# Optimization experiments

Measured on AMD Instinct MI355X. Metric: run time of the kernel, lower is better.

Reference implementation:

```python
import jax, jax.numpy as jnp
import numpy as np

N_NODES = 50000
N_EVENTS = 500000
P = 127          # previous_embed_size
A = P + 1        # agg_features
O = A + P        # w2 out size = 255
BN_EPS = 1e-5


def setup_inputs() -> dict:
    key = jax.random.key(0)
    ks = jax.random.split(key, 12)
    inp = {
        "u": jax.random.randint(ks[0], (N_EVENTS,), 0, N_NODES),
        "v": jax.random.randint(ks[1], (N_EVENTS,), 0, N_NODES),
        "g": jax.random.uniform(ks[2], (N_EVENTS, 1), dtype=jnp.float32),
        "h": jax.random.normal(ks[3], (N_NODES, P), dtype=jnp.float32),
        "remember_u": jax.random.normal(ks[4], (N_EVENTS, P), dtype=jnp.float32),
        "remember_v": jax.random.normal(ks[5], (N_EVENTS, P), dtype=jnp.float32),
        "bn_gamma": jnp.ones((A,), jnp.float32),
        "bn_beta": jnp.zeros((A,), jnp.float32),
        "w1_w": jax.random.normal(ks[6], (A, A), dtype=jnp.float32) / np.sqrt(A),
        "w1_b": jax.random.normal(ks[7], (A,), dtype=jnp.float32) * 0.01,
        "w2_w": jax.random.normal(ks[8], (O, O), dtype=jnp.float32) / np.sqrt(O),
        "w2_b": jax.random.normal(ks[9], (O,), dtype=jnp.float32) * 0.01,
        "event": N_EVENTS,
    }
    return inp


def reference(u, v, g, h, remember_u, remember_v, bn_gamma, bn_beta,
              w1_w, w1_b, w2_w, w2_b, event):
    n_nodes = h.shape[0]
    agg_feat = bn_gamma.shape[0]
    # per-edge messages: cat(stale embedding, time feature)  -> [E, A]
    src_u = jnp.concatenate([remember_u, g], axis=1)
    src_v = jnp.concatenate([remember_v, g], axis=1)
    # scatter_add into node buffers (row-wise scatter, index expanded in torch)
    agg_v = jnp.zeros((n_nodes, agg_feat), g.dtype).at[v].add(src_u)
    agg_u = jnp.zeros((n_nodes, agg_feat), g.dtype).at[u].add(src_v)
    agg = agg_u + agg_v  # [N, A]
    # BatchNorm1d (training mode: batch stats over node dim, biased var)
    mean = jnp.mean(agg, axis=0)
    var = jnp.var(agg, axis=0)
    x = (agg - mean) * jax.lax.rsqrt(var + BN_EPS) * bn_gamma + bn_beta
    # 2-layer MLP with skip-cat of h
    x1 = jax.nn.relu(x @ w1_w.T + w1_b)                 # [N, A]
    out = jnp.concatenate([h, x1], axis=1) @ w2_w.T + w2_b  # [N, A+P]
    return out
```

## Files before the change

### kernel.cpp

```cpp
#include <hip/hip_runtime.h>

constexpr int PDIM = 127;
constexpr int ADIM = 128;
constexpr int ODIM = 255;
constexpr int RTILE = 32;
constexpr int CAP = 80;
constexpr float EPS = 1e-5f;

constexpr int XS_STRIDE = 136;
constexpr int CS_STRIDE = 264;

typedef short bf16x8 __attribute__((ext_vector_type(8)));
typedef float f32x4 __attribute__((ext_vector_type(4)));

__device__ inline unsigned short f2b(float x) {
    unsigned u = __builtin_bit_cast(unsigned, x);
    u += 0x7FFF + ((u >> 16) & 1);
    return (unsigned short)(u >> 16);
}

__global__ __launch_bounds__(256) void bucket_kernel(
    const int* __restrict__ u, const int* __restrict__ v,
    const float* __restrict__ g,
    int* __restrict__ cnt, int* __restrict__ bucket,
    float* __restrict__ gsum, int E)
{
    int e = blockIdx.x * 256 + threadIdx.x;
    if (e >= E) return;
    float gv = g[e];
    int vn = v[e];
    int slot = atomicAdd(&cnt[vn], 1);
    if (slot < CAP) bucket[(long long)vn * CAP + slot] = e;
    unsafeAtomicAdd(&gsum[vn], gv);
    int un = u[e];
    slot = atomicAdd(&cnt[un], 1);
    if (slot < CAP) bucket[(long long)un * CAP + slot] = e | (1 << 20);
    unsafeAtomicAdd(&gsum[un], gv);
}

__global__ __launch_bounds__(256) void gather_kernel(
    const int* __restrict__ cnt, const int* __restrict__ bucket,
    const float* __restrict__ gsum,
    const float* __restrict__ ru, const float* __restrict__ rv,
    float* __restrict__ agg, int N)
{
    __shared__ int codes[8][CAP];
    int tid = threadIdx.x;
    int hw = tid >> 5;
    int sub = tid & 31;
    long long node = (long long)blockIdx.x * 8 + hw;
    bool valid = (node < N);
    int nd = valid ? (int)node : 0;
    int deg = valid ? cnt[nd] : 0;
    if (deg > CAP) deg = CAP;
    const int* bkt = bucket + (long long)nd * CAP;
    codes[hw][sub] = bkt[sub];
    codes[hw][32 + sub] = bkt[32 + sub];
    if (sub < CAP - 64) codes[hw][64 + sub] = bkt[64 + sub];

    int eoff = (sub < 31) ? 4 * sub : 123;
    f32x4 acc = {0.f, 0.f, 0.f, 0.f};
    int d = 0;
    for (; d + 4 <= deg; d += 4) {
        f32x4 vb[4];
        #pragma unroll
        for (int k = 0; k < 4; ++k) {
            int c = codes[hw][d + k];
            int e = c & 0xFFFFF;
            const float* s = (c & (1 << 20)) ? rv : ru;
            vb[k] = *reinterpret_cast<const f32x4*>(s + (long long)e * PDIM + eoff);
        }
        #pragma unroll
        for (int k = 0; k < 4; ++k) acc += vb[k];
    }
    for (; d < deg; ++d) {
        int c = codes[hw][d];
        int e = c & 0xFFFFF;
        const float* s = (c & (1 << 20)) ? rv : ru;
        acc += *reinterpret_cast<const f32x4*>(s + (long long)e * PDIM + eoff);
    }
    if (!valid) return;
    float* arow = agg + node * ADIM;
    if (sub < 31) {
        *reinterpret_cast<f32x4*>(arow + 4 * sub) = acc;
    } else {
        f32x4 o; o.x = acc.y; o.y = acc.z; o.z = acc.w; o.w = gsum[nd];
        *reinterpret_cast<f32x4*>(arow + 124) = o;
    }
}

__global__ __launch_bounds__(256) void colstats_kernel(
    const float* __restrict__ agg, float* __restrict__ csum,
    float* __restrict__ csumsq, int N)
{
    int j = threadIdx.x & 127;
    int rh = threadIdx.x >> 7;
    float s = 0.f, ss = 0.f;
    for (int r = blockIdx.x * 2 + rh; r < N; r += gridDim.x * 2) {
        float x = agg[(long long)r * ADIM + j];
        s += x; ss += x * x;
    }
    __shared__ float sh[2][128];
    __shared__ float sh2[2][128];
    sh[rh][j] = s; sh2[rh][j] = ss;
    __syncthreads();
    if (threadIdx.x < 128) {
        unsafeAtomicAdd(&csum[j], sh[0][j] + sh[1][j]);
        unsafeAtomicAdd(&csumsq[j], sh2[0][j] + sh2[1][j]);
    }
}

__global__ void finalize_kernel(const float* __restrict__ csum,
                                const float* __restrict__ csumsq,
                                const float* __restrict__ gamma,
                                const float* __restrict__ beta,
                                float* __restrict__ scale,
                                float* __restrict__ shift, int N)
{
    int j = threadIdx.x;
    if (j >= ADIM) return;
    float inv = 1.f / (float)N;
    float mean = csum[j] * inv;
    float var = csumsq[j] * inv - mean * mean;
    float sc = gamma[j] * rsqrtf(var + EPS);
    scale[j] = sc;
    shift[j] = beta[j] - mean * sc;
}

__global__ __launch_bounds__(256) void wprep_kernel(
    const float* __restrict__ w1, const float* __restrict__ w2,
    unsigned short* __restrict__ w1b, unsigned short* __restrict__ w2b)
{
    int t = blockIdx.x * 256 + threadIdx.x;
    if (t < 65536) {
        int o = t >> 8, k = t & 255;
        w2b[t] = (o < ODIM && k < ODIM) ? f2b(w2[o * ODIM + k]) : (unsigned short)0;
    } else {
        int s = t - 65536;
        if (s < ADIM * ADIM) w1b[s] = f2b(w1[s]);
    }
}

__global__ __launch_bounds__(256, 4) void mlp_kernel(
    const float* __restrict__ agg, const float* __restrict__ h,
    const float* __restrict__ scale, const float* __restrict__ shift,
    const unsigned short* __restrict__ w1b, const float* __restrict__ b1,
    const unsigned short* __restrict__ w2b, const float* __restrict__ b2,
    float* __restrict__ out, int N)
{
    __shared__ unsigned short xs[RTILE * XS_STRIDE];
    __shared__ unsigned short cs[RTILE * CS_STRIDE];
    int tid = threadIdx.x;
    int row0 = blockIdx.x * RTILE;
    int lane = tid & 63;
    int wave = tid >> 6;

    {
        int j = tid & 127, rh = tid >> 7;
        float sc = scale[j], sf = shift[j];
        for (int i = 0; i < RTILE / 2; ++i) {
            int r = i * 2 + rh;
            long long grow = row0 + r;
            float x = 0.f, hv = 0.f;
            if (grow < N) {
                x = agg[grow * ADIM + j] * sc + sf;
                if (j < PDIM) hv = h[grow * PDIM + j];
            }
            xs[r * XS_STRIDE + j] = f2b(x);
            cs[r * CS_STRIDE + j] = f2b(hv);
        }
        if (tid < RTILE) cs[tid * CS_STRIDE + 255] = 0;
    }
    __syncthreads();

    {
        int arow = lane & 15, akg = lane >> 4;
        bf16x8 afr[2][4];
        #pragma unroll
        for (int rt = 0; rt < 2; ++rt)
            #pragma unroll
            for (int ks = 0; ks < 4; ++ks)
                afr[rt][ks] = *reinterpret_cast<const bf16x8*>(
                    &xs[(rt * 16 + arow) * XS_STRIDE + ks * 32 + akg * 8]);
        #pragma unroll
        for (int t = 0; t < 2; ++t) {
            int bcol = (wave * 2 + t) * 16 + (lane & 15);
            bf16x8 bfr[4];
            #pragma unroll
            for (int ks = 0; ks < 4; ++ks)
                bfr[ks] = *reinterpret_cast<const bf16x8*>(&w1b[bcol * ADIM + ks * 32 + akg * 8]);
            float bias = b1[bcol];
            #pragma unroll
            for (int rt = 0; rt < 2; ++rt) {
                f32x4 acc = {0.f, 0.f, 0.f, 0.f};
                #pragma unroll
                for (int ks = 0; ks < 4; ++ks)
                    acc = __builtin_amdgcn_mfma_f32_16x16x32_bf16(afr[rt][ks], bfr[ks], acc, 0, 0, 0);
                #pragma unroll
                for (int i = 0; i < 4; ++i) {
                    int r = rt * 16 + (lane >> 4) * 4 + i;
                    float x1 = fmaxf(acc[i] + bias, 0.f);
                    cs[r * CS_STRIDE + PDIM + bcol] = f2b(x1);
                }
            }
        }
    }
    __syncthreads();

    {
        int arow = lane & 15, akg = lane >> 4;
        bf16x8 caf[2][8];
        #pragma unroll
        for (int rt = 0; rt < 2; ++rt)
            #pragma unroll
            for (int ks = 0; ks < 8; ++ks)
                caf[rt][ks] = *reinterpret_cast<const bf16x8*>(
                    &cs[(rt * 16 + arow) * CS_STRIDE + ks * 32 + akg * 8]);
        #pragma unroll
        for (int t = 0; t < 4; ++t) {
            int o = (wave * 4 + t) * 16 + (lane & 15);
            bf16x8 bfr[8];
            #pragma unroll
            for (int ks = 0; ks < 8; ++ks)
                bfr[ks] = *reinterpret_cast<const bf16x8*>(&w2b[o * 256 + ks * 32 + akg * 8]);
            float bias = (o < ODIM) ? b2[o] : 0.f;
            #pragma unroll
            for (int rt = 0; rt < 2; ++rt) {
                f32x4 acc = {0.f, 0.f, 0.f, 0.f};
                #pragma unroll
                for (int ks = 0; ks < 8; ++ks)
                    acc = __builtin_amdgcn_mfma_f32_16x16x32_bf16(caf[rt][ks], bfr[ks], acc, 0, 0, 0);
                if (o < ODIM) {
                    #pragma unroll
                    for (int i = 0; i < 4; ++i) {
                        long long grow = row0 + rt * 16 + (lane >> 4) * 4 + i;
                        if (grow < N) out[grow * ODIM + o] = acc[i] + bias;
                    }
                }
            }
        }
    }
}

extern "C" void kernel_launch(void* const* d_in, const int* in_sizes, int n_in,
                              void* d_out, int out_size, void* d_ws, size_t ws_size,
                              hipStream_t stream)
{
    const int*   u     = (const int*)d_in[0];
    const int*   v     = (const int*)d_in[1];
    const float* g     = (const float*)d_in[2];
    const float* h     = (const float*)d_in[3];
    const float* ru    = (const float*)d_in[4];
    const float* rv    = (const float*)d_in[5];
    const float* gamma = (const float*)d_in[6];
    const float* beta  = (const float*)d_in[7];
    const float* w1w   = (const float*)d_in[8];
    const float* w1b_f = (const float*)d_in[9];
    const float* w2w   = (const float*)d_in[10];
    const float* w2b_f = (const float*)d_in[11];

    int E = in_sizes[0];
    int N = in_sizes[3] / PDIM;

    int*   cnt    = (int*)d_ws;
    float* gsum   = (float*)d_ws + N;
    float* csum   = gsum + N;
    float* csumsq = csum + ADIM;
    float* scale  = csumsq + ADIM;
    float* shift  = scale + ADIM;
    int*   bucket = (int*)(shift + ADIM);
    float* agg    = (float*)(bucket + (long long)N * CAP);
    unsigned short* w1b = (unsigned short*)(agg + (long long)N * ADIM);
    unsigned short* w2b = w1b + ADIM * ADIM;

    (void)hipMemsetAsync(cnt, 0, ((size_t)(2 * N) + 2 * ADIM) * sizeof(float), stream);

    wprep_kernel<<<(65536 + ADIM * ADIM + 255) / 256, 256, 0, stream>>>(w1w, w2w, w1b, w2b);

    bucket_kernel<<<(E + 255) / 256, 256, 0, stream>>>(u, v, g, cnt, bucket, gsum, E);

    int gblocks = (N + 7) / 8;
    gather_kernel<<<gblocks, 256, 0, stream>>>(cnt, bucket, gsum, ru, rv, agg, N);

    colstats_kernel<<<1024, 256, 0, stream>>>(agg, csum, csumsq, N);
    finalize_kernel<<<1, 128, 0, stream>>>(csum, csumsq, gamma, beta, scale, shift, N);

    int mblocks = (N + RTILE - 1) / RTILE;
    mlp_kernel<<<mblocks, 256, 0, stream>>>(agg, h, scale, shift, w1b, w1b_f, w2b, w2b_f,
                                            (float*)d_out, N);
}
```

Before: 326.4 us.

## Fuse BatchNorm column statistics into gather and gather time feature per node

Column sum and sum-of-squares are now computed in the gather kernel's epilogue from register values via shared-memory reduction and atomics, removing the separate colstats pass that reread the aggregated matrix. The per-node time-feature sum is now gathered from g inside the gather loop instead of using float atomics in the bucket kernel, which also shrinks the memset. The trade-off is many more global atomics on only 256 addresses (one set per 8-node block) and an extra scattered load per edge on one lane.

```diff
diff --git a/kernel.cpp b/kernel.cpp
--- a/kernel.cpp
+++ b/kernel.cpp
@@ -21,30 +21,28 @@
 
 __global__ __launch_bounds__(256) void bucket_kernel(
     const int* __restrict__ u, const int* __restrict__ v,
-    const float* __restrict__ g,
-    int* __restrict__ cnt, int* __restrict__ bucket,
-    float* __restrict__ gsum, int E)
+    int* __restrict__ cnt, int* __restrict__ bucket, int E)
 {
     int e = blockIdx.x * 256 + threadIdx.x;
     if (e >= E) return;
-    float gv = g[e];
     int vn = v[e];
     int slot = atomicAdd(&cnt[vn], 1);
     if (slot < CAP) bucket[(long long)vn * CAP + slot] = e;
-    unsafeAtomicAdd(&gsum[vn], gv);
     int un = u[e];
     slot = atomicAdd(&cnt[un], 1);
     if (slot < CAP) bucket[(long long)un * CAP + slot] = e | (1 << 20);
-    unsafeAtomicAdd(&gsum[un], gv);
 }
 
 __global__ __launch_bounds__(256) void gather_kernel(
     const int* __restrict__ cnt, const int* __restrict__ bucket,
-    const float* __restrict__ gsum,
+    const float* __restrict__ g,
     const float* __restrict__ ru, const float* __restrict__ rv,
-    float* __restrict__ agg, int N)
+    float* __restrict__ agg, float* __restrict__ csum,
+    float* __restrict__ csumsq, int N)
 {
     __shared__ int codes[8][CAP];
+    __shared__ float ssum[8][128];
+    __shared__ float ssq[8][128];
     int tid = threadIdx.x;
     int hw = tid >> 5;
     int sub = tid & 31;
@@ -60,53 +58,63 @@
 
     int eoff = (sub < 31) ? 4 * sub : 123;
     f32x4 acc = {0.f, 0.f, 0.f, 0.f};
+    float gacc = 0.f;
+    bool g31 = (sub == 31);
     int d = 0;
     for (; d + 4 <= deg; d += 4) {
         f32x4 vb[4];
+        float gb[4];
         #pragma unroll
         for (int k = 0; k < 4; ++k) {
             int c = codes[hw][d + k];
             int e = c & 0xFFFFF;
             const float* s = (c & (1 << 20)) ? rv : ru;
             vb[k] = *reinterpret_cast<const f32x4*>(s + (long long)e * PDIM + eoff);
-        }
-        #pragma unroll
-        for (int k = 0; k < 4; ++k) acc += vb[k];
+            gb[k] = g31 ? g[e] : 0.f;
+        }
+        #pragma unroll
+        for (int k = 0; k < 4; ++k) { acc += vb[k]; gacc += gb[k]; }
     }
     for (; d < deg; ++d) {
         int c = codes[hw][d];
         int e = c & 0xFFFFF;
         const float* s = (c & (1 << 20)) ? rv : ru;
         acc += *reinterpret_cast<const f32x4*>(s + (long long)e * PDIM + eoff);
-    }
-    if (!valid) return;
-    float* arow = agg + node * ADIM;
-    if (sub < 31) {
-        *reinterpret_cast<f32x4*>(arow + 4 * sub) = acc;
+        if (g31) gacc += g[e];
+    }
+
+    int cbase = (sub < 31) ? 4 * sub : 124;
+    float v0 = (sub < 31) ? acc.x : acc.y;
+    float v1 = (sub < 31) ? acc.y : acc.z;
+    float v2 = (sub < 31) ? acc.z : acc.w;
+    float v3 = (sub < 31) ? acc.w : gacc;
+    ssum[hw][cbase + 0] = v0;  ssq[hw][cbase + 0] = v0 * v0;
+    ssum[hw][cbase + 1] = v1;  ssq[hw][cbase + 1] = v1 * v1;
+    ssum[hw][cbase + 2] = v2;  ssq[hw][cbase + 2] = v2 * v2;
+    ssum[hw][cbase + 3] = v3;  ssq[hw][cbase + 3] = v3 * v3;
+
+    if (valid) {
+        float* arow = agg + node * ADIM;
+        if (sub < 31) {
+            *reinterpret_cast<f32x4*>(arow + 4 * sub) = acc;
+        } else {
+            f32x4 o; o.x = acc.y; o.y = acc.z; o.z = acc.w; o.w = gacc;
+            *reinterpret_cast<f32x4*>(arow + 124) = o;
+        }
+    }
+
+    __syncthreads();
+    if (tid < 128) {
+        float s = 0.f;
+        #pragma unroll
+        for (int h2 = 0; h2 < 8; ++h2) s += ssum[h2][tid];
+        unsafeAtomicAdd(&csum[tid], s);
     } else {
-        f32x4 o; o.x = acc.y; o.y = acc.z; o.z = acc.w; o.w = gsum[nd];
-        *reinterpret_cast<f32x4*>(arow + 124) = o;
-    }
-}
-
-__global__ __launch_bounds__(256) void colstats_kernel(
-    const float* __restrict__ agg, float* __restrict__ csum,
-    float* __restrict__ csumsq, int N)
-{
-    int j = threadIdx.x & 127;
-    int rh = threadIdx.x >> 7;
-    float s = 0.f, ss = 0.f;
-    for (int r = blockIdx.x * 2 + rh; r < N; r += gridDim.x * 2) {
-        float x = agg[(long long)r * ADIM + j];
-        s += x; ss += x * x;
-    }
-    __shared__ float sh[2][128];
-    __shared__ float sh2[2][128];
-    sh[rh][j] = s; sh2[rh][j] = ss;
-    __syncthreads();
-    if (threadIdx.x < 128) {
-        unsafeAtomicAdd(&csum[j], sh[0][j] + sh[1][j]);
-        unsafeAtomicAdd(&csumsq[j], sh2[0][j] + sh2[1][j]);
+        int c = tid - 128;
+        float s = 0.f;
+        #pragma unroll
+        for (int h2 = 0; h2 < 8; ++h2) s += ssq[h2][c];
+        unsafeAtomicAdd(&csumsq[c], s);
     }
 }
 
@@ -263,8 +271,7 @@
     int N = in_sizes[3] / PDIM;
 
     int*   cnt    = (int*)d_ws;
-    float* gsum   = (float*)d_ws + N;
-    float* csum   = gsum + N;
+    float* csum   = (float*)d_ws + N;
     float* csumsq = csum + ADIM;
     float* scale  = csumsq + ADIM;
     float* shift  = scale + ADIM;
@@ -273,16 +280,16 @@
     unsigned short* w1b = (unsigned short*)(agg + (long long)N * ADIM);
     unsigned short* w2b = w1b + ADIM * ADIM;
 
-    (void)hipMemsetAsync(cnt, 0, ((size_t)(2 * N) + 2 * ADIM) * sizeof(float), stream);
+    (void)hipMemsetAsync(cnt, 0, ((size_t)N + 2 * ADIM) * sizeof(float), stream);
 
     wprep_kernel<<<(65536 + ADIM * ADIM + 255) / 256, 256, 0, stream>>>(w1w, w2w, w1b, w2b);
 
-    bucket_kernel<<<(E + 255) / 256, 256, 0, stream>>>(u, v, g, cnt, bucket, gsum, E);
+    bucket_kernel<<<(E + 255) / 256, 256, 0, stream>>>(u, v, cnt, bucket, E);
 
     int gblocks = (N + 7) / 8;
-    gather_kernel<<<gblocks, 256, 0, stream>>>(cnt, bucket, gsum, ru, rv, agg, N);
-
-    colstats_kernel<<<1024, 256, 0, stream>>>(agg, csum, csumsq, N);
+    gather_kernel<<<gblocks, 256, 0, stream>>>(cnt, bucket, g, ru, rv,
+                                               agg, csum, csumsq, N);
+
     finalize_kernel<<<1, 128, 0, stream>>>(csum, csumsq, gamma, beta, scale, shift, N);
 
     int mblocks = (N + RTILE - 1) / RTILE;
```

New measurement: 318.2 us. 2.5% less time.
